# Performance work log

Hardware: AMD Instinct MI355X
Metric: run time of the kernel (lower is better)

## Reference

```python
import jax, jax.numpy as jnp
import numpy as np

RES = 128          # image / k-space resolution
DECIMATION = 4     # acceleration factor
P = RES * RES // DECIMATION  # 4096 trajectory points
B = 8              # batch


def setup_inputs() -> dict:
    key = jax.random.key(0)
    k1, k2 = jax.random.split(key)
    k_space_input = jax.random.normal(k1, (B, 1, RES, RES, 2), dtype=jnp.float32)
    # learnable k-space trajectory in pixel units, range [-RES/2, RES/2]
    trajectory = (jax.random.uniform(k2, (P, 2), dtype=jnp.float32) - 0.5) * RES
    return {"k_space_input": k_space_input, "trajectory": trajectory}


def _grid_sample_points(img, pts_norm):
    """torch.nn.functional.grid_sample (bilinear, zero padding, align_corners=False)
    evaluated at a list of points.
    img: (B, C, H, W); pts_norm: (P, 2) in [-1, 1], [:, 0] -> x (W axis), [:, 1] -> y (H axis).
    Returns (B, C, P)."""
    H, W = img.shape[-2], img.shape[-1]
    x = (pts_norm[:, 0] + 1.0) * (W * 0.5) - 0.5
    y = (pts_norm[:, 1] + 1.0) * (H * 0.5) - 0.5
    x0f = jnp.floor(x)
    y0f = jnp.floor(y)
    wx = x - x0f  # differentiable interpolation weights
    wy = y - y0f
    x0 = x0f.astype(jnp.int32)
    y0 = y0f.astype(jnp.int32)

    def tap(ix, iy, w):
        valid = ((ix >= 0) & (ix < W) & (iy >= 0) & (iy < H)).astype(img.dtype)
        ixc = jnp.clip(ix, 0, W - 1)
        iyc = jnp.clip(iy, 0, H - 1)
        return img[:, :, iyc, ixc] * (w * valid)  # (B, C, P)

    return (tap(x0, y0, (1 - wx) * (1 - wy))
            + tap(x0 + 1, y0, wx * (1 - wy))
            + tap(x0, y0 + 1, (1 - wx) * wy)
            + tap(x0 + 1, y0 + 1, wx * wy))


def _forward(k_space_input, trajectory):
    # (B,1,H,W,2) -> (B,2,H,W): channels = (real, imag)
    ksp = jnp.transpose(k_space_input, (0, 1, 4, 2, 3))[:, 0]
    # bilinear resampling of cartesian k-space at the trajectory points
    pts = trajectory / (RES * 0.5)  # normalize to [-1, 1] as in the torch helper
    sub = _grid_sample_points(ksp, pts)            # (B, 2, P)
    c = sub[:, 0] + 1j * sub[:, 1]                 # complex measurements (B, P)
    # adjoint (type-1) NUFFT back to a centered RES x RES image grid:
    # img[y, x] = (1/RES) * sum_p c[p] * exp(+2*pi*i*(ky_p*y + kx_p*x)/RES)
    xs = jnp.arange(RES, dtype=jnp.float32) - RES * 0.5  # centered grid coords
    phase = (2.0 * jnp.pi / RES)
    Ax = jnp.exp(1j * phase * trajectory[:, 0][:, None] * xs[None, :])  # (P, W)
    Ay = jnp.exp(1j * phase * trajectory[:, 1][:, None] * xs[None, :])  # (P, H)
    tmp = c[:, :, None] * Ay[None, :, :]           # (B, P, H)
    img = jnp.einsum('bph,pw->bhw', tmp, Ax) / RES  # (B, H, W), 1/sqrt(H*W) scale
    out = jnp.stack([img.real, img.imag], axis=-1)[:, None]  # (B, 1, H, W, 2)
    return out


def reference(k_space_input, trajectory):
    return _forward(k_space_input, trajectory)
```

## Files before the change

kernel.cpp:

```cpp
#include <hip/hip_runtime.h>

#define RES    128
#define P_PTS  4096
#define BATCH  8
#define PHASE  0.04908738521234052f
#define CHUNKS 32

#define CB_OFF   0u
#define BT_OFF   262144u
#define AT_OFF   2359296u
#define PART_OFF 19136512u

typedef _Float16 half8  __attribute__((ext_vector_type(8)));
typedef _Float16 half2v __attribute__((ext_vector_type(2)));
typedef float    f32x4  __attribute__((ext_vector_type(4)));

__device__ __forceinline__ void gload16(const void* g, void* lbase, int lane) {
#if defined(__has_builtin) && __has_builtin(__builtin_amdgcn_global_load_lds)
    __builtin_amdgcn_global_load_lds(
        (const __attribute__((address_space(1))) void*)g,
        (__attribute__((address_space(3))) void*)lbase, 16, 0, 0);
#else
    *(float4*)((char*)lbase + lane * 16) = *(const float4*)g;
#endif
}

__global__ __launch_bounds__(256) void prep1_kernel(const float* __restrict__ ksp,
                                                    const float* __restrict__ traj,
                                                    float* __restrict__ cb,
                                                    _Float16* __restrict__ Bt) {
    const int idx = blockIdx.x * 256 + threadIdx.x;
    if (blockIdx.x < 512) {
        const int n  = idx & 127;
        const int k8 = idx >> 7;
        const float xs = (float)n - 64.0f;
        half8 v;
#pragma unroll
        for (int q = 0; q < 4; ++q) {
            const int p = k8 * 4 + q;
            float s, c;
            __sincosf(PHASE * traj[2 * p] * xs, &s, &c);
            v[2 * q]     = (_Float16)c;
            v[2 * q + 1] = (_Float16)s;
        }
        *(half8*)(Bt + (size_t)idx * 8) = v;
    } else {
        const int j = idx - 512 * 256;
        const int p = j >> 3;
        const int b = j & 7;
        const float tx = traj[2 * p], ty = traj[2 * p + 1];
        const float x = tx + 63.5f, y = ty + 63.5f;
        const float x0f = floorf(x), y0f = floorf(y);
        const float wx = x - x0f, wy = y - y0f;
        const int ix0 = (int)x0f, iy0 = (int)y0f;
        float re = 0.0f, im = 0.0f;
#pragma unroll
        for (int dy = 0; dy < 2; ++dy) {
#pragma unroll
            for (int dx = 0; dx < 2; ++dx) {
                const int ix = ix0 + dx, iy = iy0 + dy;
                const float w = (dx ? wx : 1.0f - wx) * (dy ? wy : 1.0f - wy);
                if (ix >= 0 && ix < RES && iy >= 0 && iy < RES) {
                    const int base = ((b * RES + iy) * RES + ix) * 2;
                    re = fmaf(ksp[base],     w, re);
                    im = fmaf(ksp[base + 1], w, im);
                }
            }
        }
        cb[p * 16 + 2 * b]     = re * (1.0f / 128.0f);
        cb[p * 16 + 2 * b + 1] = im * (1.0f / 128.0f);
    }
}

__global__ __launch_bounds__(256) void prepA_kernel(const float* __restrict__ traj,
                                                    const float* __restrict__ cb,
                                                    _Float16* __restrict__ At) {
    const int idx  = blockIdx.x * 256 + threadIdx.x;
    const int m_in = idx & 127;
    const int k8   = (idx >> 7) & 1023;
    const int b    = idx >> 17;
    const float hs = (float)m_in - 64.0f;
    half8 v;
#pragma unroll
    for (int q = 0; q < 4; ++q) {
        const int p = k8 * 4 + q;
        const float cr = cb[p * 16 + 2 * b];
        const float ci = cb[p * 16 + 2 * b + 1];
        float s, c;
        __sincosf(PHASE * traj[2 * p + 1] * hs, &s, &c);
        v[2 * q]     = (_Float16)(cr * c - ci * s);
        v[2 * q + 1] = (_Float16)(cr * s + ci * c);
    }
    *(half8*)(At + (size_t)idx * 8) = v;
}

__global__ __launch_bounds__(256) void gemm_kernel(const _Float16* __restrict__ At,
                                                   const _Float16* __restrict__ Bt,
                                                   half2v* __restrict__ part) {
    __shared__ __align__(16) _Float16 sA[2][8192];
    __shared__ __align__(16) _Float16 sB[2][8192];

    const int chunk = blockIdx.x;
    const int mb    = blockIdx.y;
    const int tid   = threadIdx.x;
    const int wave  = tid >> 6;
    const int lane  = tid & 63;
    const int l15   = lane & 15;
    const int q     = lane >> 4;
    const int wm    = wave >> 1;
    const int wn    = wave & 1;

    const _Float16* aBase = At + (size_t)(mb * 1024 + chunk * 32) * 1024;
    const _Float16* bBase = Bt + (size_t)(chunk * 32) * 1024;

    const half8 SGN = {(_Float16)1.f, (_Float16)-1.f, (_Float16)1.f, (_Float16)-1.f,
                       (_Float16)1.f, (_Float16)-1.f, (_Float16)1.f, (_Float16)-1.f};

    f32x4 accR[4][4], accI[4][4];
#pragma unroll
    for (int i = 0; i < 4; ++i)
#pragma unroll
        for (int j = 0; j < 4; ++j) {
            accR[i][j] = (f32x4){0.f, 0.f, 0.f, 0.f};
            accI[i][j] = (f32x4){0.f, 0.f, 0.f, 0.f};
        }

    auto stage = [&](int r, int buf) {
        const _Float16* ga = aBase + r * 8192 + wave * 2048 + lane * 8;
        const _Float16* gb = bBase + r * 8192 + wave * 2048 + lane * 8;
        _Float16* la = &sA[buf][wave * 2048];
        _Float16* lb = &sB[buf][wave * 2048];
#pragma unroll
        for (int i = 0; i < 4; ++i) {
            gload16(ga + i * 512, la + i * 512, lane);
            gload16(gb + i * 512, lb + i * 512, lane);
        }
    };

    auto compute = [&](int buf) {
#pragma unroll
        for (int s = 0; s < 2; ++s) {
            const _Float16* pa = &sA[buf][(s * 4 + q) * 1024];
            const _Float16* pb = &sB[buf][(s * 4 + q) * 1024];
            half8 an[4], bv[4], a1[4], a2[4];
#pragma unroll
            for (int t = 0; t < 4; ++t) {
                an[t] = *(const half8*)(pa + (wm * 64 + t * 16 + l15) * 8);
                bv[t] = *(const half8*)(pb + (wn * 64 + t * 16 + l15) * 8);
            }
#pragma unroll
            for (int t = 0; t < 4; ++t) {
                a1[t] = an[t] * SGN;
                a2[t] = __builtin_shufflevector(an[t], an[t],
                                                1, 0, 3, 2, 5, 4, 7, 6);
            }
#pragma unroll
            for (int mt = 0; mt < 4; ++mt)
#pragma unroll
                for (int nt = 0; nt < 4; ++nt) {
                    accR[mt][nt] = __builtin_amdgcn_mfma_f32_16x16x32_f16(
                        a1[mt], bv[nt], accR[mt][nt], 0, 0, 0);
                    accI[mt][nt] = __builtin_amdgcn_mfma_f32_16x16x32_f16(
                        a2[mt], bv[nt], accI[mt][nt], 0, 0, 0);
                }
        }
    };

    stage(0, 0);
#pragma unroll
    for (int r = 0; r < 4; ++r) {
        if (r < 3) {
            stage(r + 1, (r + 1) & 1);
            asm volatile("s_waitcnt vmcnt(8) lgkmcnt(0)\n\ts_barrier" ::: "memory");
        } else {
            asm volatile("s_waitcnt vmcnt(0) lgkmcnt(0)\n\ts_barrier" ::: "memory");
        }
        compute(r & 1);
        asm volatile("s_waitcnt lgkmcnt(0)\n\ts_barrier" ::: "memory");
    }

#pragma unroll
    for (int mt = 0; mt < 4; ++mt) {
#pragma unroll
        for (int nt = 0; nt < 4; ++nt) {
            const int n = wn * 64 + nt * 16 + l15;
#pragma unroll
            for (int rg = 0; rg < 4; ++rg) {
                const int m = mb * 128 + wm * 64 + mt * 16 + q * 4 + rg;
                half2v pv;
                pv[0] = (_Float16)accR[mt][nt][rg];
                pv[1] = (_Float16)accI[mt][nt][rg];
                part[(size_t)chunk * 131072 + m * 128 + n] = pv;
            }
        }
    }
}

__global__ __launch_bounds__(256) void reduce_kernel(const half2v* __restrict__ part,
                                                     float2* __restrict__ out) {
    const int i = blockIdx.x * 256 + threadIdx.x;
    float sr = 0.f, si = 0.f;
#pragma unroll
    for (int c = 0; c < CHUNKS; ++c) {
        half2v v = part[(size_t)c * 131072 + i];
        sr += (float)v[0];
        si += (float)v[1];
    }
    out[i] = make_float2(sr, si);
}

extern "C" void kernel_launch(void* const* d_in, const int* in_sizes, int n_in,
                              void* d_out, int out_size, void* d_ws, size_t ws_size,
                              hipStream_t stream) {
    const float* ksp  = (const float*)d_in[0];
    const float* traj = (const float*)d_in[1];

    float*     cb   = (float*)((char*)d_ws + CB_OFF);
    _Float16*  Bt   = (_Float16*)((char*)d_ws + BT_OFF);
    _Float16*  At   = (_Float16*)((char*)d_ws + AT_OFF);
    half2v*    part = (half2v*)((char*)d_ws + PART_OFF);

    hipLaunchKernelGGL(prep1_kernel,  dim3(640),        dim3(256), 0, stream,
                       ksp, traj, cb, Bt);
    hipLaunchKernelGGL(prepA_kernel,  dim3(4096),       dim3(256), 0, stream,
                       traj, cb, At);
    hipLaunchKernelGGL(gemm_kernel,   dim3(CHUNKS, 8),  dim3(256), 0, stream,
                       At, Bt, part);
    hipLaunchKernelGGL(reduce_kernel, dim3(512),        dim3(256), 0, stream,
                       part, (float2*)d_out);
}
```

Before: 83.43 us.

## Fuse prep kernels, use revolution-based sincos, retile GEMM with fewer K-chunks

Merges the two preparation kernels into one per-k8 block kernel that computes the gridded samples into shared memory and then writes both the Ax and the c*Ay fp16 operands. This removes a launch and the intermediate cb round trip. Phases are computed in revolutions with hardware sin/cos after range reduction. The GEMM is retiled to 64x128 output tiles per block with 16 K-chunks instead of 32, which halves the partial-sum buffer that the reduce kernel must read, at the cost of longer per-block K loops.

```diff
diff --git a/kernel.cpp b/kernel.cpp
--- a/kernel.cpp
+++ b/kernel.cpp
@@ -3,51 +3,39 @@
 #define RES    128
 #define P_PTS  4096
 #define BATCH  8
-#define PHASE  0.04908738521234052f
-#define CHUNKS 32
-
-#define CB_OFF   0u
-#define BT_OFF   262144u
-#define AT_OFF   2359296u
-#define PART_OFF 19136512u
+#define CHUNKS 16
+
+#define BT_OFF   0u
+#define AT_OFF   (2u * 1024u * 1024u)
+#define PART_OFF (18u * 1024u * 1024u)
 
 typedef _Float16 half8  __attribute__((ext_vector_type(8)));
 typedef _Float16 half2v __attribute__((ext_vector_type(2)));
 typedef float    f32x4  __attribute__((ext_vector_type(4)));
 
-__device__ __forceinline__ void gload16(const void* g, void* lbase, int lane) {
-#if defined(__has_builtin) && __has_builtin(__builtin_amdgcn_global_load_lds)
+__device__ __forceinline__ float2 phasor(float rev) {
+    const float f = rev - floorf(rev);
+    return make_float2(__builtin_amdgcn_cosf(f), __builtin_amdgcn_sinf(f));
+}
+
+__device__ __forceinline__ void gload16(const void* g, void* lbase) {
     __builtin_amdgcn_global_load_lds(
         (const __attribute__((address_space(1))) void*)g,
         (__attribute__((address_space(3))) void*)lbase, 16, 0, 0);
-#else
-    *(float4*)((char*)lbase + lane * 16) = *(const float4*)g;
-#endif
-}
-
-__global__ __launch_bounds__(256) void prep1_kernel(const float* __restrict__ ksp,
-                                                    const float* __restrict__ traj,
-                                                    float* __restrict__ cb,
-                                                    _Float16* __restrict__ Bt) {
-    const int idx = blockIdx.x * 256 + threadIdx.x;
-    if (blockIdx.x < 512) {
-        const int n  = idx & 127;
-        const int k8 = idx >> 7;
-        const float xs = (float)n - 64.0f;
-        half8 v;
-#pragma unroll
-        for (int q = 0; q < 4; ++q) {
-            const int p = k8 * 4 + q;
-            float s, c;
-            __sincosf(PHASE * traj[2 * p] * xs, &s, &c);
-            v[2 * q]     = (_Float16)c;
-            v[2 * q + 1] = (_Float16)s;
-        }
-        *(half8*)(Bt + (size_t)idx * 8) = v;
-    } else {
-        const int j = idx - 512 * 256;
-        const int p = j >> 3;
-        const int b = j & 7;
+}
+
+__global__ __launch_bounds__(128) void prep_kernel(const float* __restrict__ ksp,
+                                                   const float* __restrict__ traj,
+                                                   _Float16* __restrict__ Bt,
+                                                   _Float16* __restrict__ At) {
+    const int k8 = blockIdx.x;
+    const int t  = threadIdx.x;
+
+    __shared__ float2 sc[4][8];
+
+    if (t < 32) {
+        const int j = t >> 3, b = t & 7;
+        const int p = k8 * 4 + j;
         const float tx = traj[2 * p], ty = traj[2 * p + 1];
         const float x = tx + 63.5f, y = ty + 63.5f;
         const float x0f = floorf(x), y0f = floorf(y);
@@ -67,97 +55,100 @@
                 }
             }
         }
-        cb[p * 16 + 2 * b]     = re * (1.0f / 128.0f);
-        cb[p * 16 + 2 * b + 1] = im * (1.0f / 128.0f);
-    }
-}
-
-__global__ __launch_bounds__(256) void prepA_kernel(const float* __restrict__ traj,
-                                                    const float* __restrict__ cb,
-                                                    _Float16* __restrict__ At) {
-    const int idx  = blockIdx.x * 256 + threadIdx.x;
-    const int m_in = idx & 127;
-    const int k8   = (idx >> 7) & 1023;
-    const int b    = idx >> 17;
-    const float hs = (float)m_in - 64.0f;
-    half8 v;
-#pragma unroll
-    for (int q = 0; q < 4; ++q) {
-        const int p = k8 * 4 + q;
-        const float cr = cb[p * 16 + 2 * b];
-        const float ci = cb[p * 16 + 2 * b + 1];
-        float s, c;
-        __sincosf(PHASE * traj[2 * p + 1] * hs, &s, &c);
-        v[2 * q]     = (_Float16)(cr * c - ci * s);
-        v[2 * q + 1] = (_Float16)(cr * s + ci * c);
-    }
-    *(half8*)(At + (size_t)idx * 8) = v;
+        sc[j][b] = make_float2(re * (1.0f / 128.0f), im * (1.0f / 128.0f));
+    }
+    __syncthreads();
+
+    const float xs = ((float)t - 64.0f) * (1.0f / 128.0f);
+    float2 ay[4];
+    half8 bv;
+#pragma unroll
+    for (int j = 0; j < 4; ++j) {
+        const int p = k8 * 4 + j;
+        const float2 ax = phasor(traj[2 * p] * xs);
+        ay[j] = phasor(traj[2 * p + 1] * xs);
+        bv[2 * j]     = (_Float16)ax.x;
+        bv[2 * j + 1] = (_Float16)ax.y;
+    }
+    *(half8*)(Bt + ((size_t)k8 * 128 + t) * 8) = bv;
+
+#pragma unroll
+    for (int b = 0; b < 8; ++b) {
+        half8 v;
+#pragma unroll
+        for (int j = 0; j < 4; ++j) {
+            const float cr = sc[j][b].x, ci = sc[j][b].y;
+            v[2 * j]     = (_Float16)(cr * ay[j].x - ci * ay[j].y);
+            v[2 * j + 1] = (_Float16)(cr * ay[j].y + ci * ay[j].x);
+        }
+        *(half8*)(At + (((size_t)b * 1024 + k8) * 128 + t) * 8) = v;
+    }
 }
 
 __global__ __launch_bounds__(256) void gemm_kernel(const _Float16* __restrict__ At,
                                                    const _Float16* __restrict__ Bt,
                                                    half2v* __restrict__ part) {
-    __shared__ __align__(16) _Float16 sA[2][8192];
+    __shared__ __align__(16) _Float16 sA[2][4096];
     __shared__ __align__(16) _Float16 sB[2][8192];
 
     const int chunk = blockIdx.x;
-    const int mb    = blockIdx.y;
-    const int tid   = threadIdx.x;
-    const int wave  = tid >> 6;
-    const int lane  = tid & 63;
-    const int l15   = lane & 15;
-    const int q     = lane >> 4;
-    const int wm    = wave >> 1;
-    const int wn    = wave & 1;
-
-    const _Float16* aBase = At + (size_t)(mb * 1024 + chunk * 32) * 1024;
-    const _Float16* bBase = Bt + (size_t)(chunk * 32) * 1024;
+    const int mt_   = blockIdx.y;
+    const int b  = mt_ >> 1;
+    const int mh = mt_ & 1;
+    const int tid  = threadIdx.x;
+    const int wave = tid >> 6;
+    const int lane = tid & 63;
+    const int l15  = lane & 15;
+    const int q    = lane >> 4;
+
+    const _Float16* aCh = At + ((size_t)b * 1024 + chunk * 64) * 1024 + mh * 512;
+    const _Float16* bCh = Bt + (size_t)chunk * 64 * 1024;
 
     const half8 SGN = {(_Float16)1.f, (_Float16)-1.f, (_Float16)1.f, (_Float16)-1.f,
                        (_Float16)1.f, (_Float16)-1.f, (_Float16)1.f, (_Float16)-1.f};
 
-    f32x4 accR[4][4], accI[4][4];
+    f32x4 accR[4][2], accI[4][2];
 #pragma unroll
     for (int i = 0; i < 4; ++i)
 #pragma unroll
-        for (int j = 0; j < 4; ++j) {
+        for (int j = 0; j < 2; ++j) {
             accR[i][j] = (f32x4){0.f, 0.f, 0.f, 0.f};
             accI[i][j] = (f32x4){0.f, 0.f, 0.f, 0.f};
         }
 
     auto stage = [&](int r, int buf) {
-        const _Float16* ga = aBase + r * 8192 + wave * 2048 + lane * 8;
-        const _Float16* gb = bBase + r * 8192 + wave * 2048 + lane * 8;
-        _Float16* la = &sA[buf][wave * 2048];
-        _Float16* lb = &sB[buf][wave * 2048];
-#pragma unroll
-        for (int i = 0; i < 4; ++i) {
-            gload16(ga + i * 512, la + i * 512, lane);
-            gload16(gb + i * 512, lb + i * 512, lane);
+#pragma unroll
+        for (int i = 0; i < 2; ++i) {
+            const int k8l = wave * 2 + i;
+            const size_t k8o = (size_t)(r * 8 + k8l) * 1024;
+            gload16(aCh + k8o + lane * 8, &sA[buf][k8l * 512]);
+            gload16(bCh + k8o + lane * 8, &sB[buf][k8l * 1024]);
+            gload16(bCh + k8o + 512 + lane * 8, &sB[buf][k8l * 1024 + 512]);
         }
     };
 
     auto compute = [&](int buf) {
 #pragma unroll
         for (int s = 0; s < 2; ++s) {
-            const _Float16* pa = &sA[buf][(s * 4 + q) * 1024];
+            const _Float16* pa = &sA[buf][(s * 4 + q) * 512];
             const _Float16* pb = &sB[buf][(s * 4 + q) * 1024];
-            half8 an[4], bv[4], a1[4], a2[4];
-#pragma unroll
-            for (int t = 0; t < 4; ++t) {
-                an[t] = *(const half8*)(pa + (wm * 64 + t * 16 + l15) * 8);
-                bv[t] = *(const half8*)(pb + (wn * 64 + t * 16 + l15) * 8);
+            half8 an[4], bv[2], a1[4], a2[4];
+#pragma unroll
+            for (int mt = 0; mt < 4; ++mt)
+                an[mt] = *(const half8*)(pa + (mt * 16 + l15) * 8);
+#pragma unroll
+            for (int nt = 0; nt < 2; ++nt)
+                bv[nt] = *(const half8*)(pb + (wave * 32 + nt * 16 + l15) * 8);
+#pragma unroll
+            for (int mt = 0; mt < 4; ++mt) {
+                a1[mt] = an[mt] * SGN;
+                a2[mt] = __builtin_shufflevector(an[mt], an[mt],
+                                                 1, 0, 3, 2, 5, 4, 7, 6);
             }
 #pragma unroll
-            for (int t = 0; t < 4; ++t) {
-                a1[t] = an[t] * SGN;
-                a2[t] = __builtin_shufflevector(an[t], an[t],
-                                                1, 0, 3, 2, 5, 4, 7, 6);
-            }
-#pragma unroll
             for (int mt = 0; mt < 4; ++mt)
 #pragma unroll
-                for (int nt = 0; nt < 4; ++nt) {
+                for (int nt = 0; nt < 2; ++nt) {
                     accR[mt][nt] = __builtin_amdgcn_mfma_f32_16x16x32_f16(
                         a1[mt], bv[nt], accR[mt][nt], 0, 0, 0);
                     accI[mt][nt] = __builtin_amdgcn_mfma_f32_16x16x32_f16(
@@ -168,12 +159,12 @@
 
     stage(0, 0);
 #pragma unroll
-    for (int r = 0; r < 4; ++r) {
-        if (r < 3) {
+    for (int r = 0; r < 8; ++r) {
+        if (r < 7) {
             stage(r + 1, (r + 1) & 1);
-            asm volatile("s_waitcnt vmcnt(8) lgkmcnt(0)\n\ts_barrier" ::: "memory");
+            asm volatile("s_waitcnt vmcnt(6)\n\ts_barrier" ::: "memory");
         } else {
-            asm volatile("s_waitcnt vmcnt(0) lgkmcnt(0)\n\ts_barrier" ::: "memory");
+            asm volatile("s_waitcnt vmcnt(0)\n\ts_barrier" ::: "memory");
         }
         compute(r & 1);
         asm volatile("s_waitcnt lgkmcnt(0)\n\ts_barrier" ::: "memory");
@@ -182,11 +173,11 @@
 #pragma unroll
     for (int mt = 0; mt < 4; ++mt) {
 #pragma unroll
-        for (int nt = 0; nt < 4; ++nt) {
-            const int n = wn * 64 + nt * 16 + l15;
+        for (int nt = 0; nt < 2; ++nt) {
+            const int n = wave * 32 + nt * 16 + l15;
 #pragma unroll
             for (int rg = 0; rg < 4; ++rg) {
-                const int m = mb * 128 + wm * 64 + mt * 16 + q * 4 + rg;
+                const int m = b * 128 + mh * 64 + mt * 16 + q * 4 + rg;
                 half2v pv;
                 pv[0] = (_Float16)accR[mt][nt][rg];
                 pv[1] = (_Float16)accI[mt][nt][rg];
@@ -215,17 +206,14 @@
     const float* ksp  = (const float*)d_in[0];
     const float* traj = (const float*)d_in[1];
 
-    float*     cb   = (float*)((char*)d_ws + CB_OFF);
-    _Float16*  Bt   = (_Float16*)((char*)d_ws + BT_OFF);
-    _Float16*  At   = (_Float16*)((char*)d_ws + AT_OFF);
-    half2v*    part = (half2v*)((char*)d_ws + PART_OFF);
-
-    hipLaunchKernelGGL(prep1_kernel,  dim3(640),        dim3(256), 0, stream,
-                       ksp, traj, cb, Bt);
-    hipLaunchKernelGGL(prepA_kernel,  dim3(4096),       dim3(256), 0, stream,
-                       traj, cb, At);
-    hipLaunchKernelGGL(gemm_kernel,   dim3(CHUNKS, 8),  dim3(256), 0, stream,
+    _Float16* Bt   = (_Float16*)((char*)d_ws + BT_OFF);
+    _Float16* At   = (_Float16*)((char*)d_ws + AT_OFF);
+    half2v*   part = (half2v*)((char*)d_ws + PART_OFF);
+
+    hipLaunchKernelGGL(prep_kernel,   dim3(1024),        dim3(128), 0, stream,
+                       ksp, traj, Bt, At);
+    hipLaunchKernelGGL(gemm_kernel,   dim3(CHUNKS, 16),  dim3(256), 0, stream,
                        At, Bt, part);
-    hipLaunchKernelGGL(reduce_kernel, dim3(512),        dim3(256), 0, stream,
+    hipLaunchKernelGGL(reduce_kernel, dim3(512),         dim3(256), 0, stream,
                        part, (float2*)d_out);
 }
```

Result: faster. 79.64 us (-4.5%).
